# Performance work log

Measured on AMD Instinct MI355X. Metric: run time of the kernel, lower is better.

The kernel has to match this reference:

```python
import jax, jax.numpy as jnp
import numpy as np


def _min_gru_layer(h_in, Wz, bz, Wh, bh):
    # h_in: [B, T, D_in]; gates/candidate via two GEMMs
    z = jax.nn.sigmoid(jnp.einsum('btd,dh->bth', h_in, Wz) + bz)  # [B,T,H]
    h_tilde = jnp.einsum('btd,dh->bth', h_in, Wh) + bh            # [B,T,H]
    # Recurrence h_t = a_t * h_{t-1} + b_t with a_t = 1-z_t, b_t = z_t*h_tilde.
    # h_0 = 0 (frozen zeros param in the torch module), so the associative
    # scan over (a, b) directly yields h_t for t = 1..T.
    a = 1.0 - z
    b = z * h_tilde

    def combine(c1, c2):
        a1, b1 = c1
        a2, b2 = c2
        return a1 * a2, a2 * b1 + b2

    _, h = jax.lax.associative_scan(combine, (a, b), axis=1)
    return h


def setup_inputs() -> dict:
    key = jax.random.key(0)
    ks = jax.random.split(key, 8)
    B, T, Din, H, Dout = 8, 4096, 512, 1024, 512
    s_in = 1.0 / np.sqrt(Din)
    s_h = 1.0 / np.sqrt(H)
    return {
        'x':   jax.random.normal(ks[0], (B, T, Din), dtype=jnp.float32),
        'Wz0': jax.random.normal(ks[1], (Din, H), dtype=jnp.float32) * s_in,
        'bz0': jnp.zeros((H,), dtype=jnp.float32),
        'Wh0': jax.random.normal(ks[2], (Din, H), dtype=jnp.float32) * s_in,
        'bh0': jnp.zeros((H,), dtype=jnp.float32),
        'Wz1': jax.random.normal(ks[3], (H, H), dtype=jnp.float32) * s_h,
        'bz1': jnp.zeros((H,), dtype=jnp.float32),
        'Wh1': jax.random.normal(ks[4], (H, H), dtype=jnp.float32) * s_h,
        'bh1': jnp.zeros((H,), dtype=jnp.float32),
        'Wfc': jax.random.normal(ks[5], (H, Dout), dtype=jnp.float32) * s_h,
        'bfc': jnp.zeros((Dout,), dtype=jnp.float32),
    }


def reference(x, Wz0, bz0, Wh0, bh0, Wz1, bz1, Wh1, bh1, Wfc, bfc):
    h = _min_gru_layer(x, Wz0, bz0, Wh0, bh0)   # layer 0
    h = _min_gru_layer(h, Wz1, bz1, Wh1, bh1)   # layer 1
    return jnp.einsum('bth,ho->bto', h, Wfc) + bfc
```

## Files before the change

kernel.cpp:

```cpp
#include <hip/hip_runtime.h>

typedef __attribute__((ext_vector_type(4))) float fv4;
typedef __attribute__((ext_vector_type(8))) _Float16 hv8;
typedef __attribute__((ext_vector_type(4))) _Float16 hv4;
typedef __attribute__((ext_vector_type(2))) _Float16 hv2;

__device__ __forceinline__ void gload16(const void* g, void* l) {
  __builtin_amdgcn_global_load_lds(
      (const __attribute__((address_space(1))) unsigned int*)g,
      (__attribute__((address_space(3))) unsigned int*)l, 16, 0, 0);
}

struct GemmCore256 {
  const _Float16 *ap, *bp;
  size_t rstep;
  _Float16* ls;
  const _Float16 *fa, *fb;
  int wv;

  __device__ __forceinline__ void init(const _Float16* A, const _Float16* Bt,
                                       _Float16* lds, int m0, int n0, int K,
                                       int tid) {
    ls = lds;
    wv = tid >> 6;
    const int lane = tid & 63;
    const int wm = wv >> 2, wn = wv & 3;
    const int quad = lane >> 4, r = lane & 15;
    const int cg = (tid & 3) ^ ((tid >> 3) & 3);
    ap = A  + (size_t)(m0 + (tid >> 2)) * K + cg * 8;
    bp = Bt + (size_t)(n0 + (tid >> 2)) * K + cg * 8;
    rstep = (size_t)128 * K;
    const int sq = quad ^ ((r >> 1) & 3);
    fa = ls + (wm * 128 + r) * 32 + sq * 8;
    fb = ls + 8192 + (wn * 64 + r) * 32 + sq * 8;
  }

  __device__ __forceinline__ void stage4(int s) {
    _Float16* d = ls + (s & 3) * 16384 + wv * 512;
    const _Float16* a = ap + (size_t)s * 32;
    const _Float16* b = bp + (size_t)s * 32;
    gload16(a,         d);
    gload16(a + rstep, d + 4096);
    gload16(b,         d + 8192);
    gload16(b + rstep, d + 12288);
  }

  __device__ __forceinline__ void readA03(hv8 (&a)[4], int s) {
    const _Float16* fA = fa + (s & 3) * 16384;
#pragma unroll
    for (int t = 0; t < 4; ++t) a[t] = *(const hv8*)(fA + t * 512);
  }

  template <int VM, bool STAGE>
  __device__ __forceinline__ void body(fv4 acc[8][4], hv8 (&nxt)[4],
                                       hv8 (&cur)[4], int s) {
    if (STAGE) stage4(s + 3);
    if constexpr (VM >= 0)
      asm volatile("s_waitcnt vmcnt(%0)" :: "n"(VM) : "memory");
    __builtin_amdgcn_s_barrier();
    asm volatile("" ::: "memory");
    const _Float16* fA = fa + (s & 3) * 16384;
    const _Float16* fB = fb + (s & 3) * 16384;
    hv8 b0[4], a47[4];
#pragma unroll
    for (int t = 0; t < 4; ++t) b0[t] = *(const hv8*)(fB + t * 512);
#pragma unroll
    for (int t = 0; t < 4; ++t) a47[t] = *(const hv8*)(fA + (t + 4) * 512);
    readA03(nxt, s + 1);
    __builtin_amdgcn_s_setprio(1);
#pragma unroll
    for (int tm = 0; tm < 4; ++tm)
#pragma unroll
      for (int tn = 0; tn < 4; ++tn)
        acc[tm][tn] = __builtin_amdgcn_mfma_f32_16x16x32_f16(cur[tm], b0[tn],
                                                             acc[tm][tn], 0, 0, 0);
#pragma unroll
    for (int tm = 0; tm < 4; ++tm)
#pragma unroll
      for (int tn = 0; tn < 4; ++tn)
        acc[tm + 4][tn] = __builtin_amdgcn_mfma_f32_16x16x32_f16(a47[tm], b0[tn],
                                                                 acc[tm + 4][tn], 0, 0, 0);
    __builtin_amdgcn_s_setprio(0);
  }

  __device__ __forceinline__ void bodyLast(fv4 acc[8][4], hv8 (&cur)[4], int s) {
    __builtin_amdgcn_s_barrier();
    asm volatile("" ::: "memory");
    const _Float16* fA = fa + (s & 3) * 16384;
    const _Float16* fB = fb + (s & 3) * 16384;
    hv8 b0[4], a47[4];
#pragma unroll
    for (int t = 0; t < 4; ++t) b0[t] = *(const hv8*)(fB + t * 512);
#pragma unroll
    for (int t = 0; t < 4; ++t) a47[t] = *(const hv8*)(fA + (t + 4) * 512);
    __builtin_amdgcn_s_setprio(1);
#pragma unroll
    for (int tm = 0; tm < 4; ++tm)
#pragma unroll
      for (int tn = 0; tn < 4; ++tn)
        acc[tm][tn] = __builtin_amdgcn_mfma_f32_16x16x32_f16(cur[tm], b0[tn],
                                                             acc[tm][tn], 0, 0, 0);
#pragma unroll
    for (int tm = 0; tm < 4; ++tm)
#pragma unroll
      for (int tn = 0; tn < 4; ++tn)
        acc[tm + 4][tn] = __builtin_amdgcn_mfma_f32_16x16x32_f16(a47[tm], b0[tn],
                                                                 acc[tm + 4][tn], 0, 0, 0);
    __builtin_amdgcn_s_setprio(0);
  }

  __device__ __forceinline__ void run(fv4 acc[8][4], int K) {
    const int ns = K >> 5;
    stage4(0); stage4(1); stage4(2);
    asm volatile("s_waitcnt vmcnt(8)" ::: "memory");
    __builtin_amdgcn_s_barrier();
    asm volatile("" ::: "memory");
    hv8 p0[4], p1[4];
    readA03(p0, 0);
    int s = 0;
    for (; s < ns - 4; s += 2) {
      body<8, true>(acc, p1, p0, s);
      body<8, true>(acc, p0, p1, s + 1);
    }
    body<8, true >(acc, p1, p0, ns - 4);
    body<4, false>(acc, p0, p1, ns - 3);
    body<0, false>(acc, p1, p0, ns - 2);
    bodyLast(acc, p1, ns - 1);
  }
};

__device__ __forceinline__ void xcd_map(int bid, int ntl2, int mt_per_x,
                                        int& m0, int& n0) {
  const int xcd = bid & 7;
  const int k2  = bid >> 3;
  m0 = (xcd * mt_per_x + (k2 >> ntl2)) * 256;
  n0 = (k2 & ((1 << ntl2) - 1)) * 256;
}

__global__ __launch_bounds__(512, 2)
void gemm_gate(const _Float16* __restrict__ A, const _Float16* __restrict__ Btf,
               _Float16* __restrict__ zh2,
               float* __restrict__ cA, float* __restrict__ cB,
               const float* __restrict__ bz, const float* __restrict__ bh,
               int K, int ntl2, int mt_per_x) {
  __shared__ _Float16 lds[4 * 16384];
  const int tid  = threadIdx.x;
  const int lane = tid & 63;
  const int wave = tid >> 6;
  const int wm = wave >> 2, wn = wave & 3;
  const int quad = lane >> 4, r = lane & 15;
  int m0, n0;
  xcd_map(blockIdx.x, ntl2, mt_per_x, m0, n0);

  GemmCore256 core;
  core.init(A, Btf, lds, m0, n0, K, tid);
  fv4 acc[8][4] = {};
  core.run(acc, K);

  const int jb   = (n0 + wn * 64) >> 1;
  const int row0 = m0 + wm * 128 + quad * 4;
  const int cb   = (m0 >> 6) + wm * 2;
#pragma unroll
  for (int tn = 0; tn < 2; ++tn) {
    const int j = jb + tn * 16 + r;
    const float bzv = bz[j];
    const float bhv = bh[j];
#pragma unroll
    for (int tg = 0; tg < 2; ++tg) {
      float qA[4], qB[4];
#pragma unroll
      for (int tq = 0; tq < 4; ++tq) {
        const int tm = tg * 4 + tq;
        float sA = 1.0f, sB = 0.0f;
#pragma unroll
        for (int r2 = 0; r2 < 4; ++r2) {
          const float zpre = acc[tm][tn][r2] + bzv;
          const float hpre = acc[tm][tn + 2][r2] + bhv;
          const float z = 1.0f / (1.0f + __expf(-zpre));
          const _Float16 a16 = (_Float16)(1.0f - z);
          const _Float16 b16 = (_Float16)(z * hpre);
          hv2 ab = {a16, b16};
          *(hv2*)(zh2 + ((size_t)(row0 + tm * 16 + r2) * 1024 + j) * 2) = ab;
          const float af = (float)a16, bf = (float)b16;
          sB = af * sB + bf;
          sA = sA * af;
        }
        qA[tq] = sA; qB[tq] = sB;
      }
#pragma unroll
      for (int tq = 0; tq < 4; ++tq) {
        float Av = qA[tq], Bv = qB[tq];
        float Ap = __shfl_up(Av, 16, 64);
        float Bp = __shfl_up(Bv, 16, 64);
        if (quad >= 1) { Bv = Av * Bp + Bv; Av = Ap * Av; }
        Ap = __shfl_up(Av, 32, 64);
        Bp = __shfl_up(Bv, 32, 64);
        if (quad >= 2) { Bv = Av * Bp + Bv; Av = Ap * Av; }
        qA[tq] = Av; qB[tq] = Bv;
      }
      if (quad == 3) {
        float CA = 1.0f, CB = 0.0f;
#pragma unroll
        for (int tq = 0; tq < 4; ++tq) { CB = qA[tq] * CB + qB[tq]; CA *= qA[tq]; }
        cA[(size_t)(cb + tg) * 1024 + j] = CA;
        cB[(size_t)(cb + tg) * 1024 + j] = CB;
      }
    }
  }
}

__global__ __launch_bounds__(512, 2)
void gemm_f16_bt(const _Float16* __restrict__ A, const _Float16* __restrict__ Bt,
                 float* __restrict__ C, const float* __restrict__ bias,
                 int N, int K, int ntl2, int mt_per_x) {
  __shared__ _Float16 lds[4 * 16384];
  const int tid  = threadIdx.x;
  const int lane = tid & 63;
  const int wave = tid >> 6;
  const int wm = wave >> 2, wn = wave & 3;
  const int quad = lane >> 4, r = lane & 15;
  int m0, n0;
  xcd_map(blockIdx.x, ntl2, mt_per_x, m0, n0);

  GemmCore256 core;
  core.init(A, Bt, lds, m0, n0, K, tid);
  fv4 acc[8][4] = {};
  core.run(acc, K);

  const int col0 = n0 + wn * 64 + r;
  const int row0 = m0 + wm * 128 + quad * 4;
#pragma unroll
  for (int tn = 0; tn < 4; ++tn) {
    const int col = col0 + tn * 16;
    const float bs = bias[col];
#pragma unroll
    for (int tm = 0; tm < 8; ++tm) {
#pragma unroll
      for (int r2 = 0; r2 < 4; ++r2) {
        C[(size_t)(row0 + tm * 16 + r2) * N + col] = acc[tm][tn][r2] + bs;
      }
    }
  }
}

__global__ void cvt_f16(const float* __restrict__ x, _Float16* __restrict__ y) {
  size_t i = ((size_t)blockIdx.x * 256 + threadIdx.x) * 4;
  fv4 v = *(const fv4*)(x + i);
  *(hv4*)(y + i) = __builtin_convertvector(v, hv4);
}

__global__ void transpose_cvt_all(const float* __restrict__ Wz0,
                                  const float* __restrict__ Wh0,
                                  const float* __restrict__ Wz1,
                                  const float* __restrict__ Wh1,
                                  const float* __restrict__ Wfc,
                                  _Float16* __restrict__ Wzh0t,
                                  _Float16* __restrict__ Wzh1t,
                                  _Float16* __restrict__ Wft) {
  const int z = blockIdx.z;
  const float* W; _Float16* Wt; int K, N, mult, off;
  if (z == 0)      { W = Wz0; Wt = Wzh0t; K = 512;  N = 1024; mult = 64; off = 0;  }
  else if (z == 1) { W = Wh0; Wt = Wzh0t; K = 512;  N = 1024; mult = 64; off = 32; }
  else if (z == 2) { W = Wz1; Wt = Wzh1t; K = 1024; N = 1024; mult = 64; off = 0;  }
  else if (z == 3) { W = Wh1; Wt = Wzh1t; K = 1024; N = 1024; mult = 64; off = 32; }
  else             { W = Wfc; Wt = Wft;   K = 1024; N = 512;  mult = 32; off = 0;  }
  if (blockIdx.x * 32 >= (unsigned)N || blockIdx.y * 32 >= (unsigned)K) return;

  __shared__ float tile[32][33];
  const int tx = threadIdx.x, ty = threadIdx.y;
  const int n  = blockIdx.x * 32 + tx;
  const int kb = blockIdx.y * 32;
  for (int i = ty; i < 32; i += 8)
    tile[i][tx] = W[(size_t)(kb + i) * N + n];
  __syncthreads();
  const int k = kb + tx;
  for (int i = ty; i < 32; i += 8)
    Wt[(size_t)(blockIdx.x * mult + off + i) * K + k] = (_Float16)tile[tx][i];
}

__global__ void scan_phaseB(const float* __restrict__ cA, const float* __restrict__ cB,
                            float* __restrict__ hcy) {
  const int gtid = blockIdx.x * 256 + threadIdx.x;
  const int lane = gtid & 63;
  const int wid  = gtid >> 6;
  const int h  = (wid & 255) * 4;
  const int bb = wid >> 8;
  const size_t o = (size_t)(bb * 64 + lane) * 1024 + h;
  fv4 Aa = *(const fv4*)(cA + o);
  fv4 Bv = *(const fv4*)(cB + o);
#pragma unroll
  for (int d = 1; d < 64; d <<= 1) {
    fv4 Ap, Bp;
#pragma unroll
    for (int k = 0; k < 4; ++k) {
      Ap[k] = __shfl_up(Aa[k], d, 64);
      Bp[k] = __shfl_up(Bv[k], d, 64);
    }
    if (lane >= d) {
      Bv = Aa * Bp + Bv;
      Aa = Ap * Aa;
    }
  }
  fv4 hc;
#pragma unroll
  for (int k = 0; k < 4; ++k) hc[k] = __shfl_up(Bv[k], 1, 64);
  if (lane == 0) { hc.x = 0.f; hc.y = 0.f; hc.z = 0.f; hc.w = 0.f; }
  *(fv4*)(hcy + o) = hc;
}

__global__ void scan_phaseC(const _Float16* __restrict__ zh2,
                            const float* __restrict__ hcy,
                            _Float16* __restrict__ hout) {
  const int idx = blockIdx.x * 256 + threadIdx.x;
  const int h  = (idx & 255) * 4;
  const int c  = (idx >> 8) & 63;
  const int bb = idx >> 14;
  const size_t base = ((size_t)(bb * 4096 + c * 64) * 1024 + h) * 2;
  const size_t ob   = (size_t)(bb * 4096 + c * 64) * 1024 + h;
  const size_t o    = (size_t)(bb * 64 + c) * 1024 + h;
  fv4 hc = *(const fv4*)(hcy + o);
#pragma unroll 4
  for (int t = 0; t < 64; ++t) {
    hv8 v = *(const hv8*)(zh2 + base + (size_t)t * 2048);
    fv4 av = __builtin_convertvector(__builtin_shufflevector(v, v, 0, 2, 4, 6), fv4);
    fv4 bv = __builtin_convertvector(__builtin_shufflevector(v, v, 1, 3, 5, 7), fv4);
    hc = av * hc + bv;
    *(hv4*)(hout + ob + (size_t)t * 1024) = __builtin_convertvector(hc, hv4);
  }
}

extern "C" void kernel_launch(void* const* d_in, const int* in_sizes, int n_in,
                              void* d_out, int out_size, void* d_ws, size_t ws_size,
                              hipStream_t stream) {
  const float* x   = (const float*)d_in[0];
  const float* Wz0 = (const float*)d_in[1];
  const float* bz0 = (const float*)d_in[2];
  const float* Wh0 = (const float*)d_in[3];
  const float* bh0 = (const float*)d_in[4];
  const float* Wz1 = (const float*)d_in[5];
  const float* bz1 = (const float*)d_in[6];
  const float* Wh1 = (const float*)d_in[7];
  const float* bh1 = (const float*)d_in[8];
  const float* Wfc = (const float*)d_in[9];
  const float* bfc = (const float*)d_in[10];

  const int Mrows = 32768;
  const int H = 1024, Din = 512, Dout = 512;

  char* w = (char*)d_ws;
  _Float16* zh2   = (_Float16*)w; w += (size_t)Mrows * 2 * H * 2;
  _Float16* hx    = (_Float16*)w; w += (size_t)Mrows * H * 2;
  _Float16* Wzh0t = (_Float16*)w; w += (size_t)2 * H * Din * 2;
  _Float16* Wzh1t = (_Float16*)w; w += (size_t)2 * H * H * 2;
  _Float16* Wft   = (_Float16*)w; w += (size_t)Dout * H * 2;
  float*    cA    = (float*)w;    w += (size_t)8 * 64 * H * 4;
  float*    cB    = (float*)w;    w += (size_t)8 * 64 * H * 4;
  float*    hcy   = (float*)w;    w += (size_t)8 * 64 * H * 4;
  _Float16* Xb    = hx;

  cvt_f16<<<Mrows * Din / 1024, 256, 0, stream>>>(x, Xb);
  transpose_cvt_all<<<dim3(32, 32, 5), dim3(32, 8), 0, stream>>>(
      Wz0, Wh0, Wz1, Wh1, Wfc, Wzh0t, Wzh1t, Wft);

  gemm_gate<<<1024, 512, 0, stream>>>(Xb, Wzh0t, zh2, cA, cB, bz0, bh0, Din, 3, 16);
  scan_phaseB<<<512, 256, 0, stream>>>(cA, cB, hcy);
  scan_phaseC<<<512, 256, 0, stream>>>(zh2, hcy, hx);

  gemm_gate<<<1024, 512, 0, stream>>>(hx, Wzh1t, zh2, cA, cB, bz1, bh1, H, 3, 16);
  scan_phaseB<<<512, 256, 0, stream>>>(cA, cB, hcy);
  scan_phaseC<<<512, 256, 0, stream>>>(zh2, hcy, hx);

  gemm_f16_bt<<<256, 512, 0, stream>>>(hx, Wft, (float*)d_out, bfc, Dout, H, 1, 16);
}
```

Baseline: 485.2 us.

## Fuse scan carry phase into apply phase and merge input conversion into prep

Merges the fp32-to-fp16 input conversion into the weight transpose kernel, so one prep launch does both. Fuses the chunk-carry scan and the per-chunk apply into one kernel that keeps carries in LDS, removing the hcy buffer and two launches. Each block recomputes the carry scan across all hidden columns of its batch element, which multiplies cA/cB reads and shuffle work 32-fold and puts that scan ahead of the apply phase.

```diff
diff --git a/kernel.cpp b/kernel.cpp
--- a/kernel.cpp
+++ b/kernel.cpp
@@ -243,21 +243,28 @@
   }
 }
 
-__global__ void cvt_f16(const float* __restrict__ x, _Float16* __restrict__ y) {
-  size_t i = ((size_t)blockIdx.x * 256 + threadIdx.x) * 4;
-  fv4 v = *(const fv4*)(x + i);
-  *(hv4*)(y + i) = __builtin_convertvector(v, hv4);
-}
-
-__global__ void transpose_cvt_all(const float* __restrict__ Wz0,
-                                  const float* __restrict__ Wh0,
-                                  const float* __restrict__ Wz1,
-                                  const float* __restrict__ Wh1,
-                                  const float* __restrict__ Wfc,
-                                  _Float16* __restrict__ Wzh0t,
-                                  _Float16* __restrict__ Wzh1t,
-                                  _Float16* __restrict__ Wft) {
+__global__ void prep_all(const float* __restrict__ x,
+                         const float* __restrict__ Wz0,
+                         const float* __restrict__ Wh0,
+                         const float* __restrict__ Wz1,
+                         const float* __restrict__ Wh1,
+                         const float* __restrict__ Wfc,
+                         _Float16* __restrict__ Xb,
+                         _Float16* __restrict__ Wzh0t,
+                         _Float16* __restrict__ Wzh1t,
+                         _Float16* __restrict__ Wft) {
   const int z = blockIdx.z;
+  if (z >= 5) {
+    const int slot = (z - 5) * 1024 + blockIdx.y * 32 + blockIdx.x;
+    const int tid  = threadIdx.y * 32 + threadIdx.x;
+    const size_t base = (size_t)slot * 4096 + tid * 4;
+#pragma unroll
+    for (int i = 0; i < 4; ++i) {
+      fv4 v = *(const fv4*)(x + base + i * 1024);
+      *(hv4*)(Xb + base + i * 1024) = __builtin_convertvector(v, hv4);
+    }
+    return;
+  }
   const float* W; _Float16* Wt; int K, N, mult, off;
   if (z == 0)      { W = Wz0; Wt = Wzh0t; K = 512;  N = 1024; mult = 64; off = 0;  }
   else if (z == 1) { W = Wh0; Wt = Wzh0t; K = 512;  N = 1024; mult = 64; off = 32; }
@@ -278,47 +285,59 @@
     Wt[(size_t)(blockIdx.x * mult + off + i) * K + k] = (_Float16)tile[tx][i];
 }
 
-__global__ void scan_phaseB(const float* __restrict__ cA, const float* __restrict__ cB,
-                            float* __restrict__ hcy) {
-  const int gtid = blockIdx.x * 256 + threadIdx.x;
-  const int lane = gtid & 63;
-  const int wid  = gtid >> 6;
-  const int h  = (wid & 255) * 4;
-  const int bb = wid >> 8;
-  const size_t o = (size_t)(bb * 64 + lane) * 1024 + h;
-  fv4 Aa = *(const fv4*)(cA + o);
-  fv4 Bv = *(const fv4*)(cB + o);
-#pragma unroll
-  for (int d = 1; d < 64; d <<= 1) {
-    fv4 Ap, Bp;
-#pragma unroll
-    for (int k = 0; k < 4; ++k) {
-      Ap[k] = __shfl_up(Aa[k], d, 64);
-      Bp[k] = __shfl_up(Bv[k], d, 64);
-    }
-    if (lane >= d) {
-      Bv = Aa * Bp + Bv;
-      Aa = Ap * Aa;
-    }
-  }
-  fv4 hc;
-#pragma unroll
-  for (int k = 0; k < 4; ++k) hc[k] = __shfl_up(Bv[k], 1, 64);
-  if (lane == 0) { hc.x = 0.f; hc.y = 0.f; hc.z = 0.f; hc.w = 0.f; }
-  *(fv4*)(hcy + o) = hc;
-}
-
-__global__ void scan_phaseC(const _Float16* __restrict__ zh2,
-                            const float* __restrict__ hcy,
-                            _Float16* __restrict__ hout) {
-  const int idx = blockIdx.x * 256 + threadIdx.x;
-  const int h  = (idx & 255) * 4;
-  const int c  = (idx >> 8) & 63;
-  const int bb = idx >> 14;
+__global__ __launch_bounds__(512)
+void scan_fused(const float* __restrict__ cA, const float* __restrict__ cB,
+                const _Float16* __restrict__ zh2, _Float16* __restrict__ hout) {
+  __shared__ float hcyL[2][256][4];
+  const int tid  = threadIdx.x;
+  const int lane = tid & 63;
+  const int wv   = tid >> 6;
+  const int bb   = blockIdx.x >> 5;
+  const int c0   = (blockIdx.x & 31) * 2;
+
+#pragma unroll 4
+  for (int gi = 0; gi < 32; ++gi) {
+    const int g = wv * 32 + gi;
+    const size_t o = (size_t)(bb * 64 + lane) * 1024 + g * 4;
+    fv4 Aa = *(const fv4*)(cA + o);
+    fv4 Bv = *(const fv4*)(cB + o);
+#pragma unroll
+    for (int d = 1; d < 64; d <<= 1) {
+      fv4 Ap, Bp;
+#pragma unroll
+      for (int k = 0; k < 4; ++k) {
+        Ap[k] = __shfl_up(Aa[k], d, 64);
+        Bp[k] = __shfl_up(Bv[k], d, 64);
+      }
+      if (lane >= d) {
+        Bv = Aa * Bp + Bv;
+        Aa = Ap * Aa;
+      }
+    }
+    fv4 hc;
+#pragma unroll
+    for (int k = 0; k < 4; ++k) hc[k] = __shfl_up(Bv[k], 1, 64);
+    if (lane == 0) { hc.x = 0.f; hc.y = 0.f; hc.z = 0.f; hc.w = 0.f; }
+    if (lane == c0) {
+#pragma unroll
+      for (int k = 0; k < 4; ++k) hcyL[0][g][k] = hc[k];
+    }
+    if (lane == c0 + 1) {
+#pragma unroll
+      for (int k = 0; k < 4; ++k) hcyL[1][g][k] = hc[k];
+    }
+  }
+  __syncthreads();
+
+  const int ci = tid >> 8;
+  const int c  = c0 + ci;
+  const int h4 = tid & 255;
+  const int h  = h4 * 4;
   const size_t base = ((size_t)(bb * 4096 + c * 64) * 1024 + h) * 2;
   const size_t ob   = (size_t)(bb * 4096 + c * 64) * 1024 + h;
-  const size_t o    = (size_t)(bb * 64 + c) * 1024 + h;
-  fv4 hc = *(const fv4*)(hcy + o);
+  fv4 hc;
+#pragma unroll
+  for (int k = 0; k < 4; ++k) hc[k] = hcyL[ci][h4][k];
 #pragma unroll 4
   for (int t = 0; t < 64; ++t) {
     hv8 v = *(const hv8*)(zh2 + base + (size_t)t * 2048);
@@ -355,20 +374,16 @@
   _Float16* Wft   = (_Float16*)w; w += (size_t)Dout * H * 2;
   float*    cA    = (float*)w;    w += (size_t)8 * 64 * H * 4;
   float*    cB    = (float*)w;    w += (size_t)8 * 64 * H * 4;
-  float*    hcy   = (float*)w;    w += (size_t)8 * 64 * H * 4;
   _Float16* Xb    = hx;
 
-  cvt_f16<<<Mrows * Din / 1024, 256, 0, stream>>>(x, Xb);
-  transpose_cvt_all<<<dim3(32, 32, 5), dim3(32, 8), 0, stream>>>(
-      Wz0, Wh0, Wz1, Wh1, Wfc, Wzh0t, Wzh1t, Wft);
+  prep_all<<<dim3(32, 32, 9), dim3(32, 8), 0, stream>>>(
+      x, Wz0, Wh0, Wz1, Wh1, Wfc, Xb, Wzh0t, Wzh1t, Wft);
 
   gemm_gate<<<1024, 512, 0, stream>>>(Xb, Wzh0t, zh2, cA, cB, bz0, bh0, Din, 3, 16);
-  scan_phaseB<<<512, 256, 0, stream>>>(cA, cB, hcy);
-  scan_phaseC<<<512, 256, 0, stream>>>(zh2, hcy, hx);
+  scan_fused<<<256, 512, 0, stream>>>(cA, cB, zh2, hx);
 
   gemm_gate<<<1024, 512, 0, stream>>>(hx, Wzh1t, zh2, cA, cB, bz1, bh1, H, 3, 16);
-  scan_phaseB<<<512, 256, 0, stream>>>(cA, cB, hcy);
-  scan_phaseC<<<512, 256, 0, stream>>>(zh2, hcy, hx);
+  scan_fused<<<256, 512, 0, stream>>>(cA, cB, zh2, hx);
 
   gemm_f16_bt<<<256, 512, 0, stream>>>(hx, Wft, (float*)d_out, bfc, Dout, H, 1, 16);
 }
```

Measured after the change: 573.3 us. 18.2% more time.
